# Kernel optimization log

Hardware: AMD Instinct MI355X
Metric: run time of the kernel (lower is better)

## Reference

```python
import jax, jax.numpy as jnp
import numpy as np

N_ATOMS = 200_000
AVG_NEIGHBORS = 64
N_PAIRS = N_ATOMS * AVG_NEIGHBORS
BOX = 60.0  # Angstrom, so cutoff=10 masks most random pairs (realistic neighbor-list sparsity)


def setup_inputs() -> dict:
    key = jax.random.key(0)
    kR, ki, kj = jax.random.split(key, 3)
    R = jax.random.uniform(kR, (N_ATOMS, 3), dtype=jnp.float32) * BOX
    idx_i = jax.random.randint(ki, (N_PAIRS,), 0, N_ATOMS, dtype=jnp.int32)
    idx_j = jax.random.randint(kj, (N_PAIRS,), 0, N_ATOMS, dtype=jnp.int32)
    # learned scalar parameters from __init__
    epsilon = jnp.float32(0.238)
    sigma = jnp.float32(3.4)
    cutoff = jnp.float32(10.0)
    return {"R": R, "epsilon": epsilon, "sigma": sigma, "cutoff": cutoff,
            "idx_i": idx_i, "idx_j": idx_j}


def reference(R, epsilon, sigma, cutoff, idx_i, idx_j):
    """LJ 12-6 pairwise potential over a neighbor list.

    Returns (energy [N] per-atom, forces [N,3]).
    Each (i,j) pair appears in both directions in the pair list, hence the 0.5
    factor on per-atom energy; forces accumulate per direction (action-reaction
    handled by the symmetric pair list).
    """
    n_atoms = R.shape[0]
    rij = R[idx_i] - R[idx_j]                     # [P,3] gather
    r2 = jnp.sum(rij * rij, axis=-1)              # [P]
    mask = (r2 < cutoff * cutoff) & (r2 > 1e-10)  # inside cutoff, exclude coincident
    r2s = jnp.where(mask, r2, 1.0)                # safe divide
    sr2 = (sigma * sigma) / r2s
    sr6 = sr2 * sr2 * sr2
    sr12 = sr6 * sr6
    e_pair = jnp.where(mask, 4.0 * epsilon * (sr12 - sr6), 0.0)          # [P]
    f_mag = jnp.where(mask, 24.0 * epsilon * (2.0 * sr12 - sr6) / r2s, 0.0)
    f_pair = f_mag[:, None] * rij                 # [P,3]
    energy = 0.5 * jax.ops.segment_sum(e_pair, idx_i, num_segments=n_atoms)   # [N]
    forces = jax.ops.segment_sum(f_pair, idx_i, num_segments=n_atoms)         # [N,3]
    return energy, forces
```

## Files before the change

### kernel.cpp

```cpp
#include <hip/hip_runtime.h>
#include <stdint.h>


typedef int   v4i __attribute__((ext_vector_type(4)));
typedef float v4f __attribute__((ext_vector_type(4)));

#define GRP    8
#define WGT    1024
#define NWG_F  256

__global__ void __launch_bounds__(256) prep_kernel(
    const float* __restrict__ R, const float* __restrict__ cut_p,
    v4f* __restrict__ Rp, unsigned* __restrict__ packed,
    v4f* __restrict__ st, int n_atoms)
{
    int t = blockIdx.x * blockDim.x + threadIdx.x;
    int n_grp = (n_atoms + 4) / 5;
    if (t >= n_grp) return;
    const float inv_cut = 1.0f / cut_p[0];
    int a0 = t * 5;
    unsigned w = 0u;
    const v4f zero = {0.0f, 0.0f, 0.0f, 0.0f};
#pragma unroll
    for (int k = 0; k < 5; ++k) {
        int a = a0 + k;
        if (a < n_atoms) {
            float x = R[3 * a + 0];
            float y = R[3 * a + 1];
            float z = R[3 * a + 2];
            v4f v; v.x = x; v.y = y; v.z = z; v.w = 0.0f;
            Rp[a] = v;
            st[a] = zero;
            int cx = min(7, max(0, (int)(x * inv_cut)));
            int cy = min(7, max(0, (int)(y * inv_cut)));
            w |= (unsigned)(cx | (cy << 3)) << (6 * k);
        }
    }
    packed[t] = w;
}

__global__ void __launch_bounds__(256) prep_noclear_kernel(
    const float* __restrict__ R, const float* __restrict__ cut_p,
    v4f* __restrict__ Rp, unsigned* __restrict__ packed, int n_atoms)
{
    int t = blockIdx.x * blockDim.x + threadIdx.x;
    int n_grp = (n_atoms + 4) / 5;
    if (t >= n_grp) return;
    const float inv_cut = 1.0f / cut_p[0];
    int a0 = t * 5;
    unsigned w = 0u;
#pragma unroll
    for (int k = 0; k < 5; ++k) {
        int a = a0 + k;
        if (a < n_atoms) {
            float x = R[3 * a + 0];
            float y = R[3 * a + 1];
            float z = R[3 * a + 2];
            v4f v; v.x = x; v.y = y; v.z = z; v.w = 0.0f;
            Rp[a] = v;
            int cx = min(7, max(0, (int)(x * inv_cut)));
            int cy = min(7, max(0, (int)(y * inv_cut)));
            w |= (unsigned)(cx | (cy << 3)) << (6 * k);
        }
    }
    packed[t] = w;
}

__global__ void __launch_bounds__(256) pad_R_kernel(
    const float* __restrict__ R, v4f* __restrict__ Rp, int n_atoms)
{
    int a = blockIdx.x * blockDim.x + threadIdx.x;
    if (a < n_atoms) {
        v4f v;
        v.x = R[3 * a + 0];
        v.y = R[3 * a + 1];
        v.z = R[3 * a + 2];
        v.w = 0.0f;
        Rp[a] = v;
    }
}

__device__ __forceinline__ unsigned cell6w(const unsigned* __restrict__ lds32,
                                           unsigned a) {
    unsigned q = __umulhi(a, 0xCCCCCCCDu) >> 2;
    unsigned r = a - q * 5u;
    return (lds32[q] >> (r * 6u)) & 63u;
}

__device__ __forceinline__ void load_grp(
    const int* __restrict__ idx_i, const int* __restrict__ idx_j,
    int p, int n_pairs, int* __restrict__ is8, int* __restrict__ js8)
{
    if (p + GRP <= n_pairs) {
        v4i a0 = __builtin_nontemporal_load((const v4i*)idx_i + (p >> 2));
        v4i a1 = __builtin_nontemporal_load((const v4i*)idx_i + (p >> 2) + 1);
        v4i b0 = __builtin_nontemporal_load((const v4i*)idx_j + (p >> 2));
        v4i b1 = __builtin_nontemporal_load((const v4i*)idx_j + (p >> 2) + 1);
        is8[0] = a0.x; is8[1] = a0.y; is8[2] = a0.z; is8[3] = a0.w;
        is8[4] = a1.x; is8[5] = a1.y; is8[6] = a1.z; is8[7] = a1.w;
        js8[0] = b0.x; js8[1] = b0.y; js8[2] = b0.z; js8[3] = b0.w;
        js8[4] = b1.x; js8[5] = b1.y; js8[6] = b1.z; js8[7] = b1.w;
    } else {
#pragma unroll
        for (int k = 0; k < GRP; ++k) {
            bool v = (p + k < n_pairs);
            is8[k] = v ? idx_i[p + k] : 0;
            js8[k] = v ? idx_j[p + k] : 0;
        }
    }
}

__device__ __forceinline__ void filt_sel(const unsigned* __restrict__ lds32,
                                         int* __restrict__ is8,
                                         int* __restrict__ js8)
{
#pragma unroll
    for (int k = 0; k < GRP; ++k) {
        unsigned ci = cell6w(lds32, (unsigned)is8[k]);
        unsigned cj = cell6w(lds32, (unsigned)js8[k]);
        int ddx = (int)(ci & 7u) - (int)(cj & 7u);
        int ddy = (int)(ci >> 3) - (int)(cj >> 3);
        bool ok = ((unsigned)(ddx + 1) <= 2u) & ((unsigned)(ddy + 1) <= 2u);
        is8[k] = ok ? is8[k] : 0;
        js8[k] = ok ? js8[k] : 0;
    }
}

__device__ __forceinline__ void lj_body_st(
    v4f A, v4f B, float eps, float s2, float cut2, int gi,
    float* __restrict__ st)
{
    const float dx = A.x - B.x, dy = A.y - B.y, dz = A.z - B.z;
    const float r2 = dx * dx + dy * dy + dz * dz;
    if (r2 < cut2 && r2 > 1e-10f) {
        const float inv  = 1.0f / r2;
        const float sr2  = s2 * inv;
        const float sr6  = sr2 * sr2 * sr2;
        const float sr12 = sr6 * sr6;
        const float e    = 2.0f * eps * (sr12 - sr6);
        const float f    = 24.0f * eps * (2.0f * sr12 - sr6) * inv;
        float* p = st + ((size_t)(unsigned)gi << 2);
        atomicAdd(p + 0, e);
        atomicAdd(p + 1, f * dx);
        atomicAdd(p + 2, f * dy);
        atomicAdd(p + 3, f * dz);
    }
}

__device__ __forceinline__ void lj_body(
    v4f A, v4f B, float eps, float s2, float cut2, int gi,
    float* __restrict__ energy, float* __restrict__ forces)
{
    const float dx = A.x - B.x, dy = A.y - B.y, dz = A.z - B.z;
    const float r2 = dx * dx + dy * dy + dz * dz;
    if (r2 < cut2 && r2 > 1e-10f) {
        const float inv  = 1.0f / r2;
        const float sr2  = s2 * inv;
        const float sr6  = sr2 * sr2 * sr2;
        const float sr12 = sr6 * sr6;
        const float e    = 2.0f * eps * (sr12 - sr6);
        const float f    = 24.0f * eps * (2.0f * sr12 - sr6) * inv;
        atomicAdd(&energy[gi], e);
        atomicAdd(&forces[3 * gi + 0], f * dx);
        atomicAdd(&forces[3 * gi + 1], f * dy);
        atomicAdd(&forces[3 * gi + 2], f * dz);
    }
}

__global__ void __launch_bounds__(WGT, 4) lj_fused_st_kernel(
    const v4f* __restrict__ Rp,
    const unsigned* __restrict__ packed,
    const int* __restrict__ idx_i,
    const int* __restrict__ idx_j,
    const float* __restrict__ eps_p,
    const float* __restrict__ sig_p,
    const float* __restrict__ cut_p,
    float* __restrict__ st,
    int n_pairs, int pk_words, int chunk)
{
    extern __shared__ unsigned lds[];
    for (int w = threadIdx.x; w < pk_words; w += WGT)
        lds[w] = packed[w];
    __syncthreads();

    const float eps  = eps_p[0];
    const float sig  = sig_p[0];
    const float cut  = cut_p[0];
    const float s2   = sig * sig;
    const float cut2 = cut * cut;

    const int cs = blockIdx.x * chunk;
    const int ce = min(cs + chunk, n_pairs);
    const int STRIDE = WGT * GRP;

    int p0 = cs + (int)threadIdx.x * GRP;
    if (p0 >= ce) return;

    int isA[GRP], jsA[GRP], isB[GRP], jsB[GRP];

    load_grp(idx_i, idx_j, p0, n_pairs, isA, jsA);
    filt_sel(lds, isA, jsA);
    int p1 = p0 + STRIDE;

    while (true) {
        const bool h1 = p1 < ce;

        if (h1) load_grp(idx_i, idx_j, p1, n_pairs, isB, jsB);

        v4f Ri[GRP], Rj[GRP];
#pragma unroll
        for (int k = 0; k < GRP; ++k) { Ri[k] = Rp[isA[k]]; Rj[k] = Rp[jsA[k]]; }

        if (h1) filt_sel(lds, isB, jsB);

#pragma unroll
        for (int k = 0; k < GRP; ++k)
            lj_body_st(Ri[k], Rj[k], eps, s2, cut2, isA[k], st);

        if (!h1) break;
#pragma unroll
        for (int k = 0; k < GRP; ++k) { isA[k] = isB[k]; jsA[k] = jsB[k]; }
        p1 += STRIDE;
    }
}

__global__ void __launch_bounds__(256) finalize_kernel(
    const v4f* __restrict__ st, float* __restrict__ energy,
    float* __restrict__ forces, int n_atoms)
{
    int a = blockIdx.x * blockDim.x + threadIdx.x;
    if (a < n_atoms) {
        v4f s = st[a];
        energy[a]          = s.x;
        forces[3 * a + 0]  = s.y;
        forces[3 * a + 1]  = s.z;
        forces[3 * a + 2]  = s.w;
    }
}

__global__ void __launch_bounds__(WGT, 4) lj_fused_kernel(
    const v4f* __restrict__ Rp,
    const unsigned* __restrict__ packed,
    const int* __restrict__ idx_i,
    const int* __restrict__ idx_j,
    const float* __restrict__ eps_p,
    const float* __restrict__ sig_p,
    const float* __restrict__ cut_p,
    float* __restrict__ energy,
    float* __restrict__ forces,
    int n_pairs, int pk_words, int chunk)
{
    extern __shared__ unsigned lds[];
    for (int w = threadIdx.x; w < pk_words; w += WGT)
        lds[w] = packed[w];
    __syncthreads();

    const float eps  = eps_p[0];
    const float sig  = sig_p[0];
    const float cut  = cut_p[0];
    const float s2   = sig * sig;
    const float cut2 = cut * cut;

    const int cs = blockIdx.x * chunk;
    const int ce = min(cs + chunk, n_pairs);
    const int STRIDE = WGT * GRP;

    int p0 = cs + (int)threadIdx.x * GRP;
    if (p0 >= ce) return;

    int isA[GRP], jsA[GRP], isB[GRP], jsB[GRP];
    load_grp(idx_i, idx_j, p0, n_pairs, isA, jsA);
    filt_sel(lds, isA, jsA);
    int p1 = p0 + STRIDE;

    while (true) {
        const bool h1 = p1 < ce;
        if (h1) load_grp(idx_i, idx_j, p1, n_pairs, isB, jsB);
        v4f Ri[GRP], Rj[GRP];
#pragma unroll
        for (int k = 0; k < GRP; ++k) { Ri[k] = Rp[isA[k]]; Rj[k] = Rp[jsA[k]]; }
        if (h1) filt_sel(lds, isB, jsB);
#pragma unroll
        for (int k = 0; k < GRP; ++k)
            lj_body(Ri[k], Rj[k], eps, s2, cut2, isA[k], energy, forces);
        if (!h1) break;
#pragma unroll
        for (int k = 0; k < GRP; ++k) { isA[k] = isB[k]; jsA[k] = jsB[k]; }
        p1 += STRIDE;
    }
}

#define PPT 8
__global__ void __launch_bounds__(256) lj_pairs_fb_kernel(
    const v4f* __restrict__ Rp,
    const v4i* __restrict__ idx_i4, const v4i* __restrict__ idx_j4,
    const float* __restrict__ eps_p, const float* __restrict__ sig_p,
    const float* __restrict__ cut_p,
    float* __restrict__ energy, float* __restrict__ forces, int n_oct)
{
    int t = blockIdx.x * blockDim.x + threadIdx.x;
    if (t >= n_oct) return;
    const float eps  = eps_p[0];
    const float sig  = sig_p[0];
    const float cut  = cut_p[0];
    const float s2   = sig * sig;
    const float cut2 = cut * cut;
    v4i ii0 = __builtin_nontemporal_load(idx_i4 + 2 * t);
    v4i ii1 = __builtin_nontemporal_load(idx_i4 + 2 * t + 1);
    v4i jj0 = __builtin_nontemporal_load(idx_j4 + 2 * t);
    v4i jj1 = __builtin_nontemporal_load(idx_j4 + 2 * t + 1);
    int is[PPT] = { ii0.x, ii0.y, ii0.z, ii0.w, ii1.x, ii1.y, ii1.z, ii1.w };
    int js[PPT] = { jj0.x, jj0.y, jj0.z, jj0.w, jj1.x, jj1.y, jj1.z, jj1.w };
    v4f Ri[PPT], Rj[PPT];
#pragma unroll
    for (int k = 0; k < PPT; ++k) Ri[k] = Rp[is[k]];
#pragma unroll
    for (int k = 0; k < PPT; ++k) Rj[k] = Rp[js[k]];
#pragma unroll
    for (int k = 0; k < PPT; ++k)
        lj_body(Ri[k], Rj[k], eps, s2, cut2, is[k], energy, forces);
}

__global__ void lj_pairs_fb_tail_kernel(
    const v4f* __restrict__ Rp,
    const int* __restrict__ idx_i, const int* __restrict__ idx_j,
    const float* __restrict__ eps_p, const float* __restrict__ sig_p,
    const float* __restrict__ cut_p,
    float* __restrict__ energy, float* __restrict__ forces,
    int start, int n_pairs)
{
    int p = start + blockIdx.x * blockDim.x + threadIdx.x;
    if (p >= n_pairs) return;
    const float eps = eps_p[0];
    const float sig = sig_p[0];
    const float cut = cut_p[0];
    lj_body(Rp[idx_i[p]], Rp[idx_j[p]], eps, sig * sig, cut * cut,
            idx_i[p], energy, forces);
}

extern "C" void kernel_launch(void* const* d_in, const int* in_sizes, int n_in,
                              void* d_out, int out_size, void* d_ws, size_t ws_size,
                              hipStream_t stream) {
    const float* R     = (const float*)d_in[0];
    const float* eps_p = (const float*)d_in[1];
    const float* sig_p = (const float*)d_in[2];
    const float* cut_p = (const float*)d_in[3];
    const int*   idx_i = (const int*)d_in[4];
    const int*   idx_j = (const int*)d_in[5];

    const int n_atoms = in_sizes[0] / 3;
    const int n_pairs = in_sizes[4];

    float* energy = (float*)d_out;
    float* forces = (float*)d_out + n_atoms;

    char* ws = (char*)d_ws;
    const size_t rp_b     = (((size_t)n_atoms * 16) + 255) & ~(size_t)255;
    const int    pk_words = (n_atoms + 4) / 5;
    const size_t pk_b     = (((size_t)pk_words * 4) + 255) & ~(size_t)255;
    const size_t st_b     = (((size_t)n_atoms * 16) + 255) & ~(size_t)255;
    const size_t lds_b    = (((size_t)pk_words * 4) + 15) & ~(size_t)15;

    const bool have_rp  = ws_size >= rp_b;
    const bool lds_ok   = lds_b <= 160000;
    const bool use_st   = have_rp && lds_ok
                          && (ws_size >= rp_b + pk_b + st_b);
    const bool use_old  = !use_st && have_rp && lds_ok
                          && (ws_size >= rp_b + pk_b);

    v4f*      Rp     = (v4f*)ws;
    unsigned* packed = (unsigned*)(ws + rp_b);
    float*    st     = (float*)(ws + rp_b + pk_b);

    if (use_st) {
        int pblocks = (pk_words + 255) / 256;
        prep_kernel<<<pblocks, 256, 0, stream>>>(
            R, cut_p, Rp, packed, (v4f*)st, n_atoms);

        (void)hipFuncSetAttribute((const void*)lj_fused_st_kernel,
                                  hipFuncAttributeMaxDynamicSharedMemorySize,
                                  (int)lds_b);
        int chunk = (((n_pairs + NWG_F - 1) / NWG_F) + GRP - 1) & ~(GRP - 1);
        lj_fused_st_kernel<<<NWG_F, WGT, lds_b, stream>>>(
            Rp, packed, idx_i, idx_j, eps_p, sig_p, cut_p,
            st, n_pairs, pk_words, chunk);

        int fblocks = (n_atoms + 255) / 256;
        finalize_kernel<<<fblocks, 256, 0, stream>>>(
            (const v4f*)st, energy, forces, n_atoms);
    } else if (use_old) {
        (void)hipMemsetAsync(d_out, 0, (size_t)out_size * sizeof(float), stream);

        int pblocks = (pk_words + 255) / 256;
        prep_noclear_kernel<<<pblocks, 256, 0, stream>>>(
            R, cut_p, Rp, packed, n_atoms);

        (void)hipFuncSetAttribute((const void*)lj_fused_kernel,
                                  hipFuncAttributeMaxDynamicSharedMemorySize,
                                  (int)lds_b);
        int chunk = (((n_pairs + NWG_F - 1) / NWG_F) + GRP - 1) & ~(GRP - 1);
        lj_fused_kernel<<<NWG_F, WGT, lds_b, stream>>>(
            Rp, packed, idx_i, idx_j, eps_p, sig_p, cut_p,
            energy, forces, n_pairs, pk_words, chunk);
    } else if (have_rp) {
        (void)hipMemsetAsync(d_out, 0, (size_t)out_size * sizeof(float), stream);

        int blocks = (n_atoms + 255) / 256;
        pad_R_kernel<<<blocks, 256, 0, stream>>>(R, Rp, n_atoms);
        const int n_oct = n_pairs / PPT;
        const int start = n_oct * PPT;
        if (n_oct > 0) {
            int fblocks = (n_oct + 255) / 256;
            lj_pairs_fb_kernel<<<fblocks, 256, 0, stream>>>(
                Rp, (const v4i*)idx_i, (const v4i*)idx_j,
                eps_p, sig_p, cut_p, energy, forces, n_oct);
        }
        if (start < n_pairs) {
            lj_pairs_fb_tail_kernel<<<1, 64, 0, stream>>>(
                Rp, idx_i, idx_j, eps_p, sig_p, cut_p,
                energy, forces, start, n_pairs);
        }
    }
}
```

Before: 190.6 us.

## Restructure pair loop into three-stage software pipeline with 4-pair groups

Replaces the fused pair kernel's two-stage loop (index load overlapped with gather) with a three-stage pipeline: it loads and filters indices two iterations ahead, gathers positions one iteration ahead, and computes the current group. Group size per step drops from 8 to 4 pairs to keep register pressure in check, using ping-pong A/B buffers. The aim is to hide the latency of the random position gathers behind the LJ compute and atomics. In exchange it issues fewer loads per iteration, adds more loop control, and may still raise register use under the 1024-thread launch bound.

```diff
diff --git a/kernel.cpp b/kernel.cpp
--- a/kernel.cpp
+++ b/kernel.cpp
@@ -5,6 +5,7 @@
 typedef int   v4i __attribute__((ext_vector_type(4)));
 typedef float v4f __attribute__((ext_vector_type(4)));
 
+#define GRP4   4
 #define GRP    8
 #define WGT    1024
 #define NWG_F  256
@@ -87,42 +88,50 @@
     return (lds32[q] >> (r * 6u)) & 63u;
 }
 
-__device__ __forceinline__ void load_grp(
+__device__ __forceinline__ void load_grp4(
     const int* __restrict__ idx_i, const int* __restrict__ idx_j,
-    int p, int n_pairs, int* __restrict__ is8, int* __restrict__ js8)
-{
-    if (p + GRP <= n_pairs) {
-        v4i a0 = __builtin_nontemporal_load((const v4i*)idx_i + (p >> 2));
-        v4i a1 = __builtin_nontemporal_load((const v4i*)idx_i + (p >> 2) + 1);
-        v4i b0 = __builtin_nontemporal_load((const v4i*)idx_j + (p >> 2));
-        v4i b1 = __builtin_nontemporal_load((const v4i*)idx_j + (p >> 2) + 1);
-        is8[0] = a0.x; is8[1] = a0.y; is8[2] = a0.z; is8[3] = a0.w;
-        is8[4] = a1.x; is8[5] = a1.y; is8[6] = a1.z; is8[7] = a1.w;
-        js8[0] = b0.x; js8[1] = b0.y; js8[2] = b0.z; js8[3] = b0.w;
-        js8[4] = b1.x; js8[5] = b1.y; js8[6] = b1.z; js8[7] = b1.w;
+    int p, int n_pairs, int* __restrict__ is4, int* __restrict__ js4)
+{
+    if (p + GRP4 <= n_pairs) {
+        v4i a = __builtin_nontemporal_load((const v4i*)idx_i + (p >> 2));
+        v4i b = __builtin_nontemporal_load((const v4i*)idx_j + (p >> 2));
+        is4[0] = a.x; is4[1] = a.y; is4[2] = a.z; is4[3] = a.w;
+        js4[0] = b.x; js4[1] = b.y; js4[2] = b.z; js4[3] = b.w;
     } else {
 #pragma unroll
-        for (int k = 0; k < GRP; ++k) {
+        for (int k = 0; k < GRP4; ++k) {
             bool v = (p + k < n_pairs);
-            is8[k] = v ? idx_i[p + k] : 0;
-            js8[k] = v ? idx_j[p + k] : 0;
-        }
-    }
-}
-
-__device__ __forceinline__ void filt_sel(const unsigned* __restrict__ lds32,
-                                         int* __restrict__ is8,
-                                         int* __restrict__ js8)
-{
-#pragma unroll
-    for (int k = 0; k < GRP; ++k) {
-        unsigned ci = cell6w(lds32, (unsigned)is8[k]);
-        unsigned cj = cell6w(lds32, (unsigned)js8[k]);
+            is4[k] = v ? idx_i[p + k] : 0;
+            js4[k] = v ? idx_j[p + k] : 0;
+        }
+    }
+}
+
+__device__ __forceinline__ void loadz4(
+    const int* __restrict__ idx_i, const int* __restrict__ idx_j,
+    int p, int ce, int n_pairs, int* __restrict__ is4, int* __restrict__ js4)
+{
+    if (p < ce) {
+        load_grp4(idx_i, idx_j, p, n_pairs, is4, js4);
+    } else {
+#pragma unroll
+        for (int k = 0; k < GRP4; ++k) { is4[k] = 0; js4[k] = 0; }
+    }
+}
+
+__device__ __forceinline__ void filt4(const unsigned* __restrict__ lds32,
+                                      int* __restrict__ is4,
+                                      int* __restrict__ js4)
+{
+#pragma unroll
+    for (int k = 0; k < GRP4; ++k) {
+        unsigned ci = cell6w(lds32, (unsigned)is4[k]);
+        unsigned cj = cell6w(lds32, (unsigned)js4[k]);
         int ddx = (int)(ci & 7u) - (int)(cj & 7u);
         int ddy = (int)(ci >> 3) - (int)(cj >> 3);
         bool ok = ((unsigned)(ddx + 1) <= 2u) & ((unsigned)(ddy + 1) <= 2u);
-        is8[k] = ok ? is8[k] : 0;
-        js8[k] = ok ? js8[k] : 0;
+        is4[k] = ok ? is4[k] : 0;
+        js4[k] = ok ? js4[k] : 0;
     }
 }
 
@@ -167,7 +176,16 @@
     }
 }
 
-__global__ void __launch_bounds__(WGT, 4) lj_fused_st_kernel(
+#define GATHER4(IS, JS, RI, RJ)                                         \
+    _Pragma("unroll")                                                   \
+    for (int k = 0; k < GRP4; ++k) { RI[k] = Rp[IS[k]]; RJ[k] = Rp[JS[k]]; }
+
+#define COMPUTE4(RI, RJ, IS)                                            \
+    _Pragma("unroll")                                                   \
+    for (int k = 0; k < GRP4; ++k)                                      \
+        lj_body_st(RI[k], RJ[k], eps, s2, cut2, IS[k], st);
+
+__global__ void __launch_bounds__(WGT, 4) lj_fused_p3_kernel(
     const v4f* __restrict__ Rp,
     const unsigned* __restrict__ packed,
     const int* __restrict__ idx_i,
@@ -191,36 +209,52 @@
 
     const int cs = blockIdx.x * chunk;
     const int ce = min(cs + chunk, n_pairs);
-    const int STRIDE = WGT * GRP;
-
-    int p0 = cs + (int)threadIdx.x * GRP;
-    if (p0 >= ce) return;
-
-    int isA[GRP], jsA[GRP], isB[GRP], jsB[GRP];
-
-    load_grp(idx_i, idx_j, p0, n_pairs, isA, jsA);
-    filt_sel(lds, isA, jsA);
-    int p1 = p0 + STRIDE;
+    const int S  = WGT * GRP4;
+    const int pg = cs + (int)threadIdx.x * GRP4;
+    if (pg >= ce) return;
+    int remaining = (ce - cs - ((int)threadIdx.x * GRP4) + S - 1) / S;
+
+    int iA[GRP4], jA[GRP4], iB[GRP4], jB[GRP4], iT[GRP4], jT[GRP4];
+    v4f RiA[GRP4], RjA[GRP4], RiB[GRP4], RjB[GRP4];
+
+    loadz4(idx_i, idx_j, pg, ce, n_pairs, iA, jA);
+    filt4(lds, iA, jA);
+    GATHER4(iA, jA, RiA, RjA);
+    loadz4(idx_i, idx_j, pg + S, ce, n_pairs, iB, jB);
+    filt4(lds, iB, jB);
+    int pT = pg + 2 * S;
 
     while (true) {
-        const bool h1 = p1 < ce;
-
-        if (h1) load_grp(idx_i, idx_j, p1, n_pairs, isB, jsB);
-
-        v4f Ri[GRP], Rj[GRP];
-#pragma unroll
-        for (int k = 0; k < GRP; ++k) { Ri[k] = Rp[isA[k]]; Rj[k] = Rp[jsA[k]]; }
-
-        if (h1) filt_sel(lds, isB, jsB);
-
-#pragma unroll
-        for (int k = 0; k < GRP; ++k)
-            lj_body_st(Ri[k], Rj[k], eps, s2, cut2, isA[k], st);
-
-        if (!h1) break;
-#pragma unroll
-        for (int k = 0; k < GRP; ++k) { isA[k] = isB[k]; jsA[k] = jsB[k]; }
-        p1 += STRIDE;
+        {
+            const bool hB = remaining > 1;
+            if (hB) GATHER4(iB, jB, RiB, RjB);
+            const bool hT = remaining > 2;
+            if (hT) loadz4(idx_i, idx_j, pT, ce, n_pairs, iT, jT);
+            COMPUTE4(RiA, RjA, iA);
+            remaining -= 1;
+            if (remaining == 0) break;
+            if (hT) {
+                filt4(lds, iT, jT);
+#pragma unroll
+                for (int k = 0; k < GRP4; ++k) { iA[k] = iT[k]; jA[k] = jT[k]; }
+            }
+            pT += S;
+        }
+        {
+            const bool hA = remaining > 1;
+            if (hA) GATHER4(iA, jA, RiA, RjA);
+            const bool hT = remaining > 2;
+            if (hT) loadz4(idx_i, idx_j, pT, ce, n_pairs, iT, jT);
+            COMPUTE4(RiB, RjB, iB);
+            remaining -= 1;
+            if (remaining == 0) break;
+            if (hT) {
+                filt4(lds, iT, jT);
+#pragma unroll
+                for (int k = 0; k < GRP4; ++k) { iB[k] = iT[k]; jB[k] = jT[k]; }
+            }
+            pT += S;
+        }
     }
 }
 
@@ -235,6 +269,45 @@
         forces[3 * a + 0]  = s.y;
         forces[3 * a + 1]  = s.z;
         forces[3 * a + 2]  = s.w;
+    }
+}
+
+__device__ __forceinline__ void load_grp8(
+    const int* __restrict__ idx_i, const int* __restrict__ idx_j,
+    int p, int n_pairs, int* __restrict__ is8, int* __restrict__ js8)
+{
+    if (p + GRP <= n_pairs) {
+        v4i a0 = __builtin_nontemporal_load((const v4i*)idx_i + (p >> 2));
+        v4i a1 = __builtin_nontemporal_load((const v4i*)idx_i + (p >> 2) + 1);
+        v4i b0 = __builtin_nontemporal_load((const v4i*)idx_j + (p >> 2));
+        v4i b1 = __builtin_nontemporal_load((const v4i*)idx_j + (p >> 2) + 1);
+        is8[0] = a0.x; is8[1] = a0.y; is8[2] = a0.z; is8[3] = a0.w;
+        is8[4] = a1.x; is8[5] = a1.y; is8[6] = a1.z; is8[7] = a1.w;
+        js8[0] = b0.x; js8[1] = b0.y; js8[2] = b0.z; js8[3] = b0.w;
+        js8[4] = b1.x; js8[5] = b1.y; js8[6] = b1.z; js8[7] = b1.w;
+    } else {
+#pragma unroll
+        for (int k = 0; k < GRP; ++k) {
+            bool v = (p + k < n_pairs);
+            is8[k] = v ? idx_i[p + k] : 0;
+            js8[k] = v ? idx_j[p + k] : 0;
+        }
+    }
+}
+
+__device__ __forceinline__ void filt_sel8(const unsigned* __restrict__ lds32,
+                                          int* __restrict__ is8,
+                                          int* __restrict__ js8)
+{
+#pragma unroll
+    for (int k = 0; k < GRP; ++k) {
+        unsigned ci = cell6w(lds32, (unsigned)is8[k]);
+        unsigned cj = cell6w(lds32, (unsigned)js8[k]);
+        int ddx = (int)(ci & 7u) - (int)(cj & 7u);
+        int ddy = (int)(ci >> 3) - (int)(cj >> 3);
+        bool ok = ((unsigned)(ddx + 1) <= 2u) & ((unsigned)(ddy + 1) <= 2u);
+        is8[k] = ok ? is8[k] : 0;
+        js8[k] = ok ? js8[k] : 0;
     }
 }
 
@@ -269,17 +342,17 @@
     if (p0 >= ce) return;
 
     int isA[GRP], jsA[GRP], isB[GRP], jsB[GRP];
-    load_grp(idx_i, idx_j, p0, n_pairs, isA, jsA);
-    filt_sel(lds, isA, jsA);
+    load_grp8(idx_i, idx_j, p0, n_pairs, isA, jsA);
+    filt_sel8(lds, isA, jsA);
     int p1 = p0 + STRIDE;
 
     while (true) {
         const bool h1 = p1 < ce;
-        if (h1) load_grp(idx_i, idx_j, p1, n_pairs, isB, jsB);
+        if (h1) load_grp8(idx_i, idx_j, p1, n_pairs, isB, jsB);
         v4f Ri[GRP], Rj[GRP];
 #pragma unroll
         for (int k = 0; k < GRP; ++k) { Ri[k] = Rp[isA[k]]; Rj[k] = Rp[jsA[k]]; }
-        if (h1) filt_sel(lds, isB, jsB);
+        if (h1) filt_sel8(lds, isB, jsB);
 #pragma unroll
         for (int k = 0; k < GRP; ++k)
             lj_body(Ri[k], Rj[k], eps, s2, cut2, isA[k], energy, forces);
@@ -377,11 +450,11 @@
         prep_kernel<<<pblocks, 256, 0, stream>>>(
             R, cut_p, Rp, packed, (v4f*)st, n_atoms);
 
-        (void)hipFuncSetAttribute((const void*)lj_fused_st_kernel,
+        (void)hipFuncSetAttribute((const void*)lj_fused_p3_kernel,
                                   hipFuncAttributeMaxDynamicSharedMemorySize,
                                   (int)lds_b);
         int chunk = (((n_pairs + NWG_F - 1) / NWG_F) + GRP - 1) & ~(GRP - 1);
-        lj_fused_st_kernel<<<NWG_F, WGT, lds_b, stream>>>(
+        lj_fused_p3_kernel<<<NWG_F, WGT, lds_b, stream>>>(
             Rp, packed, idx_i, idx_j, eps_p, sig_p, cut_p,
             st, n_pairs, pk_words, chunk);
 
```

New measurement: 187.2 us. About the same (-1.8%).
